# Performance work log

Measured on AMD Instinct MI355X. Metric: run time of the kernel, lower is better.

Reference implementation:

```python
import jax, jax.numpy as jnp
import numpy as np

N, E, H, FE, FV, L, FL, FO = 20000, 320000, 256, 64, 64, 4, 1024, 1


def setup_inputs() -> dict:
    key = jax.random.key(0)
    ks = jax.random.split(key, 28)
    s = 0.05
    rn = lambda k, shp: jax.random.normal(k, shp, jnp.float32) * s
    inp = {
        'x': jax.random.normal(ks[0], (N, FV), jnp.float32),
        'edge_attr': jax.random.normal(ks[1], (E, FE), jnp.float32),
        'edge_index': jax.random.randint(ks[2], (2, E), 0, N, jnp.int64) if False else jax.random.randint(ks[2], (2, E), 0, N),
        'ew': rn(ks[3], (H, FE)), 'eb': rn(ks[4], (H,)),
        'vw': rn(ks[5], (H, FV)), 'vb': rn(ks[6], (H,)),
        'Le_w': rn(ks[7], (L, H, H)), 'Le_b': rn(ks[8], (L, H)),
        'Lv_w': rn(ks[9], (L, H, H)), 'Lv_b': rn(ks[10], (L, H)),
        'bne_g': jnp.ones((L, H), jnp.float32), 'bne_b': jnp.zeros((L, H), jnp.float32),
        'bnv_g': jnp.ones((L, H), jnp.float32), 'bnv_b': jnp.zeros((L, H), jnp.float32),
        'gru_wih': rn(ks[11], (L, 3 * H, H)), 'gru_whh': rn(ks[12], (L, 3 * H, H)),
        'gru_bih': rn(ks[13], (L, 3 * H)), 'gru_bhh': rn(ks[14], (L, 3 * H)),
        'fin_w': rn(ks[15], (FL, H)), 'fin_b': rn(ks[16], (FL,)),
        'out_w': rn(ks[17], (FO, FL)), 'out_b': rn(ks[18], (FO,)),
    }
    return inp


def _bn(x, g, b):
    # BatchNorm1d, training-mode batch statistics (biased variance), eps=1e-5
    m = x.mean(axis=0)
    v = x.var(axis=0)
    return (x - m) * jax.lax.rsqrt(v + 1e-5) * g + b


def _forward(x, edge_attr, edge_index, ew, eb, vw, vb, Le_w, Le_b, Lv_w, Lv_b,
             bne_g, bne_b, bnv_g, bnv_b, gru_wih, gru_whh, gru_bih, gru_bhh,
             fin_w, fin_b, out_w, out_b):
    n_nodes = x.shape[0]
    num_layers = Le_w.shape[0]
    src, dst = edge_index[0], edge_index[1]
    seg = jnp.concatenate([src, dst])  # each edge contributes to both endpoints
    e_in = edge_attr @ ew.T + eb       # [E, H]
    v_in = x @ vw.T + vb               # [N, H]
    for k in range(num_layers):
        e = e_in @ Le_w[k].T + Le_b[k]
        vp = v_in @ Lv_w[k].T + Lv_b[k]
        ep = jax.nn.relu(_bn(e + vp[src] + vp[dst], bne_g[k], bne_b[k]))  # [E, H]
        # scatter-max of incident edge features into each vertex
        vie = jax.ops.segment_max(jnp.concatenate([ep, ep], axis=0), seg,
                                  num_segments=n_nodes)
        vie = jnp.where(jnp.isfinite(vie), vie, 0.0)  # isolated vertices -> 0
        # single-step GRU: input vie, hidden v_in
        gi = vie @ gru_wih[k].T + gru_bih[k]
        gh = v_in @ gru_whh[k].T + gru_bhh[k]
        ir, iz, ig = jnp.split(gi, 3, axis=1)
        hr, hz, hg = jnp.split(gh, 3, axis=1)
        r = jax.nn.sigmoid(ir + hr)
        z = jax.nn.sigmoid(iz + hz)
        n = jnp.tanh(ig + r * hg)
        h = (1.0 - z) * n + z * v_in
        v_c = jax.nn.relu(_bn(h, bnv_g[k], bnv_b[k]))
        v_in = v_c + v_in
        e_in = ep + e_in
    e_fin = e_in @ fin_w.T + fin_b
    return e_fin @ out_w.T + out_b  # [E, 1]


def reference(x, edge_attr, edge_index, ew, eb, vw, vb, Le_w, Le_b, Lv_w, Lv_b,
              bne_g, bne_b, bnv_g, bnv_b, gru_wih, gru_whh, gru_bih, gru_bhh,
              fin_w, fin_b, out_w, out_b):
    return _forward(x, edge_attr, edge_index, ew, eb, vw, vb, Le_w, Le_b, Lv_w,
                    Lv_b, bne_g, bne_b, bnv_g, bnv_b, gru_wih, gru_whh,
                    gru_bih, gru_bhh, fin_w, fin_b, out_w, out_b)
```

## Files before the change

kernel.cpp:

```cpp
#include <hip/hip_runtime.h>
#include <stdint.h>

constexpr int N  = 20000;
constexpr int E  = 320000;
constexpr int H  = 256;
constexpr int FEAT = 64;
constexpr int NL = 4;
constexpr int FL = 1024;
constexpr int NB_E = E / 64;

typedef unsigned short u16;
typedef short bf16x8 __attribute__((ext_vector_type(8)));
typedef float f32x4 __attribute__((ext_vector_type(4)));

__device__ __forceinline__ float bf2f(u16 u) {
    union { uint32_t i; float f; } v; v.i = ((uint32_t)u) << 16; return v.f;
}
__device__ __forceinline__ u16 f2bf(float f) {
    union { uint32_t i; float f; } v; v.f = f;
    uint32_t r = v.i + 0x7FFFu + ((v.i >> 16) & 1u);
    return (u16)(r >> 16);
}
__device__ __forceinline__ float sigmf(float x) { return 1.f / (1.f + __expf(-x)); }
__device__ __forceinline__ float tanhf_(float x) { return 2.f / (1.f + __expf(-2.f * x)) - 1.f; }

__device__ __forceinline__ unsigned int encf(float x) {
    unsigned int u = __float_as_uint(x);
    return (u & 0x80000000u) ? ~u : (u | 0x80000000u);
}
__device__ __forceinline__ float decf(unsigned int k) {
    unsigned int u = (k & 0x80000000u) ? (k ^ 0x80000000u) : ~k;
    return __uint_as_float(u);
}
__device__ __forceinline__ bf16x8 addbf8(bf16x8 a, bf16x8 b) {
    bf16x8 o;
#pragma unroll
    for (int j = 0; j < 8; ++j)
        o[j] = (short)f2bf(bf2f((u16)(unsigned short)a[j]) + bf2f((u16)(unsigned short)b[j]));
    return o;
}

__device__ __forceinline__ bf16x8 ldbf(const float* wf, size_t off) {
    float4 b0 = *(const float4*)(wf + off);
    float4 b1 = *(const float4*)(wf + off + 4);
    bf16x8 r;
    r[0] = (short)f2bf(b0.x); r[1] = (short)f2bf(b0.y);
    r[2] = (short)f2bf(b0.z); r[3] = (short)f2bf(b0.w);
    r[4] = (short)f2bf(b1.x); r[5] = (short)f2bf(b1.y);
    r[6] = (short)f2bf(b1.z); r[7] = (short)f2bf(b1.w);
    return r;
}

__global__ void k_fuse_final(const float* __restrict__ fin_w, const float* __restrict__ fin_b,
                             const float* __restrict__ out_w, const float* __restrict__ out_b,
                             float* __restrict__ w_fo) {
    int h = threadIdx.x;
    float acc = 0.f;
    for (int f = 0; f < FL; ++f) acc = fmaf(out_w[f], fin_w[(size_t)f * H + h], acc);
    w_fo[h] = acc;
    if (h == 0) {
        float b = 0.f;
        for (int f = 0; f < FL; ++f) b = fmaf(out_w[f], fin_b[f], b);
        w_fo[H] = b + out_b[0];
    }
}

__global__ void k_cvt_frag(const float* __restrict__ w, u16* __restrict__ o,
                           int R, int K, int total) {
    int i = blockIdx.x * 256 + threadIdx.x;
    if (i >= total) return;
    int fpm = (R * K) >> 3;
    int m = i / fpm, f = i % fpm;
    int l16 = f & 15, qd = (f >> 4) & 3;
    int rem = f >> 6;
    int kdiv = K >> 5;
    int ks = rem % kdiv, g = rem / kdiv;
    int row = g * 16 + l16, k = ks * 32 + qd * 8;
    const float* src = w + ((size_t)m * R + row) * K + k;
    u16* dst = o + (size_t)i * 8;
    *(ushort4*)dst       = make_ushort4(f2bf(src[0]), f2bf(src[1]), f2bf(src[2]), f2bf(src[3]));
    *(ushort4*)(dst + 4) = make_ushort4(f2bf(src[4]), f2bf(src[5]), f2bf(src[6]), f2bf(src[7]));
}

__global__ void k_zero_int(int* __restrict__ p, int n) {
    int i = blockIdx.x * 256 + threadIdx.x;
    if (i < n) p[i] = 0;
}
__global__ void k_zero_f64(double* __restrict__ p, int n) {
    int i = blockIdx.x * 256 + threadIdx.x;
    if (i < n) p[i] = 0.0;
}
__global__ void k_hist2(const int* __restrict__ src, const int* __restrict__ dst,
                        int* __restrict__ curS, int* __restrict__ curD) {
    int e = blockIdx.x * 256 + threadIdx.x;
    if (e < E) { atomicAdd(&curS[src[e]], 1); atomicAdd(&curD[dst[e]], 1); }
}
__global__ void k_scan(int* __restrict__ cur) {
    __shared__ int cs[256];
    int t = threadIdx.x;
    constexpr int CH = (N + 255) / 256;
    int beg = t * CH, end = min(beg + CH, N);
    int s = 0;
    for (int i = beg; i < end; ++i) s += cur[i];
    cs[t] = s;
    __syncthreads();
    for (int off = 1; off < 256; off <<= 1) {
        int v = cs[t];
        int u = (t >= off) ? cs[t - off] : 0;
        __syncthreads();
        cs[t] = v + u;
        __syncthreads();
    }
    int run = (t > 0) ? cs[t - 1] : 0;
    for (int i = beg; i < end; ++i) { int d = cur[i]; cur[i] = run; run += d; }
}
__global__ void k_fill_perm(const int* __restrict__ src, const int* __restrict__ dst,
                            int* __restrict__ curS, int* __restrict__ curD,
                            int4* __restrict__ adjS, int4* __restrict__ sd2, int* __restrict__ pos) {
    int e = blockIdx.x * 256 + threadIdx.x;
    if (e < E) {
        int s = src[e], d = dst[e];
        int q = atomicAdd(&curD[d], 1);
        sd2[q] = make_int4(s, d, e, 0);
        pos[e] = q;
        int p = atomicAdd(&curS[s], 1);
        adjS[p] = make_int4(q, s, d, s);
    }
}
__global__ void k_fill_u32(unsigned int* __restrict__ p, unsigned int val) {
    size_t i = ((size_t)blockIdx.x * 256 + threadIdx.x) * 4;
    uint4 v = make_uint4(val, val, val, val);
    *(uint4*)(p + i) = v;
}

template <bool W16>
__global__ __launch_bounds__(256, 3) void k_proj_mfma(
    const float* __restrict__ A, const u16* __restrict__ wb, const float* __restrict__ wf,
    const float* __restrict__ bias, u16* __restrict__ C, int M, const int* __restrict__ perm)
{
    __shared__ u16 As[64][72];
    int t = threadIdx.x;
    int row0 = blockIdx.x * 64;
    int r = t >> 2, q = t & 3;
    if (row0 + r < M) {
        const float* gp = A + (size_t)(row0 + r) * FEAT + q * 16;
#pragma unroll
        for (int i = 0; i < 4; ++i) {
            float4 v = *(const float4*)(gp + i * 4);
            *(ushort4*)&As[r][q * 16 + i * 4] = make_ushort4(f2bf(v.x), f2bf(v.y), f2bf(v.z), f2bf(v.w));
        }
    } else {
#pragma unroll
        for (int i = 0; i < 4; ++i) *(ushort4*)&As[r][q * 16 + i * 4] = make_ushort4(0, 0, 0, 0);
    }
    __syncthreads();
    int w = t >> 6, l = t & 63, lane16 = l & 15, quad = l >> 4;
    f32x4 acc[4][4];
#pragma unroll
    for (int i = 0; i < 4; ++i)
#pragma unroll
        for (int j = 0; j < 4; ++j) acc[i][j] = (f32x4){0.f, 0.f, 0.f, 0.f};
    int foff = (quad * 16 + lane16) * 8;
#pragma unroll
    for (int k0 = 0; k0 < FEAT; k0 += 32) {
        int ks = k0 >> 5;
        bf16x8 a[4], b[4];
#pragma unroll
        for (int mt = 0; mt < 4; ++mt)
            a[mt] = *(const bf16x8*)&As[mt * 16 + lane16][k0 + quad * 8];
#pragma unroll
        for (int nt = 0; nt < 4; ++nt) {
            if constexpr (W16)
                b[nt] = *(const bf16x8*)(wb + (size_t)((nt * 4 + w) * 2 + ks) * 512 + foff);
            else
                b[nt] = ldbf(wf, (size_t)(w * 16 + nt * 64 + lane16) * FEAT + k0 + quad * 8);
        }
#pragma unroll
        for (int mt = 0; mt < 4; ++mt)
#pragma unroll
            for (int nt = 0; nt < 4; ++nt)
                acc[mt][nt] = __builtin_amdgcn_mfma_f32_16x16x32_bf16(a[mt], b[nt], acc[mt][nt], 0, 0, 0);
    }
#pragma unroll
    for (int nt = 0; nt < 4; ++nt) {
        int col = w * 16 + nt * 64 + lane16;
        float bv = bias[col];
#pragma unroll
        for (int mt = 0; mt < 4; ++mt)
#pragma unroll
            for (int reg = 0; reg < 4; ++reg) {
                int row = mt * 16 + quad * 4 + reg;
                if (row0 + row < M) {
                    int pr = perm ? perm[row0 + row] : row0 + row;
                    C[(size_t)pr * H + col] = f2bf(acc[mt][nt][reg] + bv);
                }
            }
    }
}

template <bool W16>
__global__ __launch_bounds__(256, 2) void k_node_mfma(
    const u16* __restrict__ A, const u16* __restrict__ wb, const float* __restrict__ wf,
    u16* __restrict__ C)
{
    __shared__ u16 As[64][264];
    int t = threadIdx.x;
    int row0 = blockIdx.x * 64;
    int rows = min(64, N - row0);
    int r = t >> 2, q = t & 3;
    if (r < rows) {
        const u16* gp = A + (size_t)(row0 + r) * H + q * 64;
#pragma unroll
        for (int i = 0; i < 8; ++i)
            *(bf16x8*)&As[r][q * 64 + i * 8] = *(const bf16x8*)(gp + i * 8);
    } else {
#pragma unroll
        for (int i = 0; i < 16; ++i) *(ushort4*)&As[r][q * 64 + i * 4] = make_ushort4(0, 0, 0, 0);
    }
    __syncthreads();
    int w = t >> 6, l = t & 63, lane16 = l & 15, quad = l >> 4;
    f32x4 acc[4][4];
#pragma unroll
    for (int i = 0; i < 4; ++i)
#pragma unroll
        for (int j = 0; j < 4; ++j) acc[i][j] = (f32x4){0.f, 0.f, 0.f, 0.f};
    int foff = (quad * 16 + lane16) * 8;
    for (int k0 = 0; k0 < H; k0 += 32) {
        int ks = k0 >> 5;
        bf16x8 a[4], b[4];
#pragma unroll
        for (int mt = 0; mt < 4; ++mt)
            a[mt] = *(const bf16x8*)&As[mt * 16 + lane16][k0 + quad * 8];
#pragma unroll
        for (int nt = 0; nt < 4; ++nt) {
            if constexpr (W16)
                b[nt] = *(const bf16x8*)(wb + (size_t)((nt * 4 + w) * 8 + ks) * 512 + foff);
            else
                b[nt] = ldbf(wf, (size_t)(w * 16 + nt * 64 + lane16) * H + k0 + quad * 8);
        }
#pragma unroll
        for (int mt = 0; mt < 4; ++mt)
#pragma unroll
            for (int nt = 0; nt < 4; ++nt)
                acc[mt][nt] = __builtin_amdgcn_mfma_f32_16x16x32_bf16(a[mt], b[nt], acc[mt][nt], 0, 0, 0);
    }
#pragma unroll
    for (int nt = 0; nt < 4; ++nt) {
        int col = w * 16 + nt * 64 + lane16;
#pragma unroll
        for (int mt = 0; mt < 4; ++mt)
#pragma unroll
            for (int reg = 0; reg < 4; ++reg) {
                int row = mt * 16 + quad * 4 + reg;
                if (row < rows)
                    C[(size_t)(row0 + row) * H + col] = f2bf(acc[mt][nt][reg]);
            }
    }
}

__global__ __launch_bounds__(512, 4) void k_edge_first(
    const u16* __restrict__ ein2, const u16* __restrict__ wsw,
    const u16* __restrict__ vp, const int4* __restrict__ sd2,
    const int* __restrict__ endo,
    unsigned int* __restrict__ vie, double* __restrict__ stats_e)
{
    __shared__ u16 As[64][264];
    __shared__ u16 Us[64][264];
    __shared__ int s_node[64];
    __shared__ int s_int[64];
    u16 (*praw)[264] = As;

    int t = threadIdx.x;
    int p0 = blockIdx.x * 64;
    int r = t >> 3, q = t & 7;
    {
        int4 en = sd2[p0 + r];
        const u16* gp = ein2 + (size_t)(p0 + r) * H + q * 32;
        const u16* vs = vp + (size_t)en.x * H + q * 32;
        const u16* vd = vp + (size_t)en.y * H + q * 32;
#pragma unroll
        for (int i = 0; i < 4; ++i)
            *(bf16x8*)&As[r][q * 32 + i * 8] = *(const bf16x8*)(gp + i * 8);
#pragma unroll
        for (int i = 0; i < 4; ++i) {
            bf16x8 a8 = *(const bf16x8*)(vs + i * 8);
            bf16x8 b8 = *(const bf16x8*)(vd + i * 8);
            *(bf16x8*)&Us[r][q * 32 + i * 8] = addbf8(a8, b8);
        }
    }
    if (t < 64) {
        int nd = sd2[p0 + t].y;
        s_node[t] = nd;
        int seg0 = p0 + (t & 32);
        int st = (nd == 0) ? 0 : endo[nd - 1];
        int ee = endo[nd];
        s_int[t] = (st >= seg0) && (ee <= seg0 + 32);
    }
    __syncthreads();

    int w = t >> 6, l = t & 63, lane16 = l & 15, quad = l >> 4;
    f32x4 acc[4][2];
#pragma unroll
    for (int i = 0; i < 4; ++i)
#pragma unroll
        for (int j = 0; j < 2; ++j) acc[i][j] = (f32x4){0.f, 0.f, 0.f, 0.f};
    int woff = (quad * 16 + lane16) * 8;
    for (int ks = 0; ks < 8; ++ks) {
        int k0 = ks * 32;
        bf16x8 a[4], b[2];
#pragma unroll
        for (int mt = 0; mt < 4; ++mt)
            a[mt] = *(const bf16x8*)&As[mt * 16 + lane16][k0 + quad * 8];
#pragma unroll
        for (int nt = 0; nt < 2; ++nt)
            b[nt] = *(const bf16x8*)(wsw + (size_t)(w * 2 + nt) * 4096 + ks * 512 + woff);
#pragma unroll
        for (int mt = 0; mt < 4; ++mt)
#pragma unroll
            for (int nt = 0; nt < 2; ++nt)
                acc[mt][nt] = __builtin_amdgcn_mfma_f32_16x16x32_bf16(a[mt], b[nt], acc[mt][nt], 0, 0, 0);
    }
    __syncthreads();

#pragma unroll
    for (int nt = 0; nt < 2; ++nt) {
        int col = w * 32 + nt * 16 + lane16;
        float s = 0.f, qq = 0.f;
#pragma unroll
        for (int mt = 0; mt < 4; ++mt)
#pragma unroll
            for (int reg = 0; reg < 4; ++reg) {
                int row = mt * 16 + quad * 4 + reg;
                float v = acc[mt][nt][reg] + bf2f(Us[row][col]);
                praw[row][col] = f2bf(v);
                s += v; qq += v * v;
            }
        s  += __shfl_xor(s, 16, 64);  s  += __shfl_xor(s, 32, 64);
        qq += __shfl_xor(qq, 16, 64); qq += __shfl_xor(qq, 32, 64);
        if (quad == 0) {
            int slice = blockIdx.x & 63;
            atomicAdd(&stats_e[(size_t)slice * 512 + col], (double)s);
            atomicAdd(&stats_e[(size_t)slice * 512 + 256 + col], (double)qq);
        }
    }
    __syncthreads();
    {
        int seg = t >> 8, col = t & 255;
        int base = seg * 32;
        int cur = s_node[base];
        float m = bf2f(praw[base][col]);
        for (int rr = 1; rr < 32; ++rr) {
            int nd = s_node[base + rr];
            float v = bf2f(praw[base + rr][col]);
            if (nd != cur) {
                if (s_int[base + rr - 1]) vie[(size_t)cur * H + col] = encf(m);
                else atomicMax(&vie[(size_t)cur * H + col], encf(m));
                cur = nd; m = v;
            } else m = fmaxf(m, v);
        }
        if (s_int[base + 31]) vie[(size_t)cur * H + col] = encf(m);
        else atomicMax(&vie[(size_t)cur * H + col], encf(m));
    }
}

__global__ __launch_bounds__(512, 4) void k_edge_second(
    const u16* __restrict__ ein2, const u16* __restrict__ wsw,
    const u16* __restrict__ vp, const int4* __restrict__ adj,
    unsigned int* __restrict__ vie,
    const float* __restrict__ scale, const float* __restrict__ shift,
    u16* __restrict__ ein_rw)
{
    __shared__ u16 As[64][264];
    __shared__ u16 Us[64][264];
    __shared__ int s_pos[64];
    __shared__ int s_node[64];
    u16 (*praw)[264] = As;

    int t = threadIdx.x;
    int p0 = blockIdx.x * 64;
    int r = t >> 3, q = t & 7;
    bf16x8 ein_reg[4];
    {
        int4 en = adj[p0 + r];
        const u16* gp = ein2 + (size_t)en.x * H + q * 32;
        const u16* vs = vp + (size_t)en.y * H + q * 32;
        const u16* vd = vp + (size_t)en.z * H + q * 32;
#pragma unroll
        for (int i = 0; i < 4; ++i) {
            ein_reg[i] = *(const bf16x8*)(gp + i * 8);
            *(bf16x8*)&As[r][q * 32 + i * 8] = ein_reg[i];
        }
#pragma unroll
        for (int i = 0; i < 4; ++i) {
            bf16x8 a8 = *(const bf16x8*)(vs + i * 8);
            bf16x8 b8 = *(const bf16x8*)(vd + i * 8);
            *(bf16x8*)&Us[r][q * 32 + i * 8] = addbf8(a8, b8);
        }
    }
    if (t < 64) {
        int4 en = adj[p0 + t];
        s_pos[t] = en.x; s_node[t] = en.w;
    }
    __syncthreads();

    int w = t >> 6, l = t & 63, lane16 = l & 15, quad = l >> 4;
    f32x4 acc[4][2];
#pragma unroll
    for (int i = 0; i < 4; ++i)
#pragma unroll
        for (int j = 0; j < 2; ++j) acc[i][j] = (f32x4){0.f, 0.f, 0.f, 0.f};
    int woff = (quad * 16 + lane16) * 8;
    for (int ks = 0; ks < 8; ++ks) {
        int k0 = ks * 32;
        bf16x8 a[4], b[2];
#pragma unroll
        for (int mt = 0; mt < 4; ++mt)
            a[mt] = *(const bf16x8*)&As[mt * 16 + lane16][k0 + quad * 8];
#pragma unroll
        for (int nt = 0; nt < 2; ++nt)
            b[nt] = *(const bf16x8*)(wsw + (size_t)(w * 2 + nt) * 4096 + ks * 512 + woff);
#pragma unroll
        for (int mt = 0; mt < 4; ++mt)
#pragma unroll
            for (int nt = 0; nt < 2; ++nt)
                acc[mt][nt] = __builtin_amdgcn_mfma_f32_16x16x32_bf16(a[mt], b[nt], acc[mt][nt], 0, 0, 0);
    }
    __syncthreads();

#pragma unroll
    for (int nt = 0; nt < 2; ++nt) {
        int col = w * 32 + nt * 16 + lane16;
#pragma unroll
        for (int mt = 0; mt < 4; ++mt)
#pragma unroll
            for (int reg = 0; reg < 4; ++reg) {
                int row = mt * 16 + quad * 4 + reg;
                praw[row][col] = f2bf(acc[mt][nt][reg] + bf2f(Us[row][col]));
            }
    }
    __syncthreads();
    {
        int seg = t >> 8, col = t & 255;
        int base = seg * 32;
        int cur = s_node[base];
        float m = bf2f(praw[base][col]);
        for (int rr = 1; rr < 32; ++rr) {
            int nd = s_node[base + rr];
            float v = bf2f(praw[base + rr][col]);
            if (nd != cur) {
                atomicMax(&vie[(size_t)cur * H + col], encf(m));
                cur = nd; m = v;
            } else m = fmaxf(m, v);
        }
        atomicMax(&vie[(size_t)cur * H + col], encf(m));
    }
    {
        u16* gp = ein_rw + (size_t)s_pos[r] * H + q * 32;
        const float* scp = scale + q * 32;
        const float* shp = shift + q * 32;
#pragma unroll
        for (int i = 0; i < 4; ++i) {
            int c = q * 32 + i * 8;
            bf16x8 pr = *(const bf16x8*)&praw[r][c];
            bf16x8 ov;
#pragma unroll
            for (int j = 0; j < 8; ++j) {
                float sc = scp[i * 8 + j];
                float sh = shp[i * 8 + j];
                float o = bf2f((u16)(unsigned short)ein_reg[i][j])
                        + fmaxf(fmaf(bf2f((u16)(unsigned short)pr[j]), sc, sh), 0.f);
                ov[j] = (short)f2bf(o);
            }
            *(bf16x8*)(gp + i * 8) = ov;
        }
    }
}

__global__ void k_bn_final_e(const double* __restrict__ stats_e,
                             const float* __restrict__ g, const float* __restrict__ b,
                             float* __restrict__ scale, float* __restrict__ shift) {
    int j = threadIdx.x;
    double m = 0.0, q = 0.0;
    for (int s = 0; s < 64; ++s) {
        m += stats_e[(size_t)s * 512 + j];
        q += stats_e[(size_t)s * 512 + 256 + j];
    }
    m /= (double)E;
    double var = q / (double)E - m * m;
    if (var < 0.0) var = 0.0;
    float inv = rsqrtf((float)var + 1e-5f);
    float sc = g[j] * inv;
    scale[j] = sc;
    shift[j] = b[j] - (float)m * sc;
}

__global__ void k_bn_final(const double* __restrict__ stats, int base,
                           const float* __restrict__ g, const float* __restrict__ b,
                           double cnt, float* __restrict__ scale, float* __restrict__ shift) {
    int j = threadIdx.x;
    double m = stats[base + j] / cnt;
    double var = stats[base + 256 + j] / cnt - m * m;
    if (var < 0.0) var = 0.0;
    float inv = rsqrtf((float)var + 1e-5f);
    float sc = g[j] * inv;
    scale[j] = sc;
    shift[j] = b[j] - (float)m * sc;
}

__global__ void k_vie_final(unsigned int* __restrict__ vie_u,
                            const float* __restrict__ scale, const float* __restrict__ shift) {
    size_t idx = ((size_t)blockIdx.x * 256 + threadIdx.x) * 4;
    int col = (int)(idx & (size_t)(H - 1));
    uint4 u = *(const uint4*)(vie_u + idx);
    float4 sc = *(const float4*)(scale + col);
    float4 sh = *(const float4*)(shift + col);
    float4 o;
    o.x = (u.x == 0u) ? 0.f : fmaxf(fmaf(decf(u.x), sc.x, sh.x), 0.f);
    o.y = (u.y == 0u) ? 0.f : fmaxf(fmaf(decf(u.y), sc.y, sh.y), 0.f);
    o.z = (u.z == 0u) ? 0.f : fmaxf(fmaf(decf(u.z), sc.z, sh.z), 0.f);
    o.w = (u.w == 0u) ? 0.f : fmaxf(fmaf(decf(u.w), sc.w, sh.w), 0.f);
    *(float4*)((float*)vie_u + idx) = o;
}

template <bool W16>
__global__ __launch_bounds__(256, 3) void k_gru_mfma(
    const float* __restrict__ vie, const u16* __restrict__ vin,
    const u16* __restrict__ wihb, const float* __restrict__ wihf,
    const u16* __restrict__ whhb, const float* __restrict__ whhf,
    const float* __restrict__ bih, const float* __restrict__ bhh,
    u16* __restrict__ hout, double* __restrict__ stats_v)
{
    __shared__ u16 Ae[32][264];
    __shared__ u16 Av[32][264];
    __shared__ float csum[256], csq[256];
    int t = threadIdx.x;
    int row0 = blockIdx.x * 32;
    int rows = min(32, N - row0);
    int r = t >> 3, q = t & 7;
    if (r < rows) {
        const float* gp = vie + (size_t)(row0 + r) * H + q * 32;
        const u16* hp = vin + (size_t)(row0 + r) * H + q * 32;
#pragma unroll
        for (int i = 0; i < 8; ++i) {
            float4 v = *(const float4*)(gp + i * 4);
            *(ushort4*)&Ae[r][q * 32 + i * 4] = make_ushort4(f2bf(v.x), f2bf(v.y), f2bf(v.z), f2bf(v.w));
        }
#pragma unroll
        for (int i = 0; i < 4; ++i)
            *(bf16x8*)&Av[r][q * 32 + i * 8] = *(const bf16x8*)(hp + i * 8);
    } else {
#pragma unroll
        for (int i = 0; i < 8; ++i) {
            *(ushort4*)&Ae[r][q * 32 + i * 4] = make_ushort4(0, 0, 0, 0);
            *(ushort4*)&Av[r][q * 32 + i * 4] = make_ushort4(0, 0, 0, 0);
        }
    }
    __syncthreads();
    int w = t >> 6, l = t & 63, lane16 = l & 15, quad = l >> 4;
    int foff = (quad * 16 + lane16) * 8;

    for (int g = 0; g < 4; ++g) {
        int j = g * 64 + w * 16 + lane16;
        f32x4 aR[2], aZ[2], aIG[2], aHG[2];
#pragma unroll
        for (int mt = 0; mt < 2; ++mt) {
            aR[mt] = (f32x4){0.f, 0.f, 0.f, 0.f};  aZ[mt] = (f32x4){0.f, 0.f, 0.f, 0.f};
            aIG[mt] = (f32x4){0.f, 0.f, 0.f, 0.f}; aHG[mt] = (f32x4){0.f, 0.f, 0.f, 0.f};
        }
        for (int k0 = 0; k0 < H; k0 += 32) {
            bf16x8 ae[2], av[2];
#pragma unroll
            for (int mt = 0; mt < 2; ++mt) {
                ae[mt] = *(const bf16x8*)&Ae[mt * 16 + lane16][k0 + quad * 8];
                av[mt] = *(const bf16x8*)&Av[mt * 16 + lane16][k0 + quad * 8];
            }
            bf16x8 bri, bzi, bgi, brh, bzh, bgh;
            if constexpr (W16) {
                size_t fo = ((size_t)(g * 4 + w) * 8 + (k0 >> 5)) * 512 + foff;
                bri = *(const bf16x8*)(wihb + fo);
                bzi = *(const bf16x8*)(wihb + 65536 + fo);
                bgi = *(const bf16x8*)(wihb + 131072 + fo);
                brh = *(const bf16x8*)(whhb + fo);
                bzh = *(const bf16x8*)(whhb + 65536 + fo);
                bgh = *(const bf16x8*)(whhb + 131072 + fo);
            } else {
                size_t kq = (size_t)k0 + quad * 8;
                bri = ldbf(wihf, (size_t)j * H + kq);
                bzi = ldbf(wihf, (size_t)(H + j) * H + kq);
                bgi = ldbf(wihf, (size_t)(2 * H + j) * H + kq);
                brh = ldbf(whhf, (size_t)j * H + kq);
                bzh = ldbf(whhf, (size_t)(H + j) * H + kq);
                bgh = ldbf(whhf, (size_t)(2 * H + j) * H + kq);
            }
#pragma unroll
            for (int mt = 0; mt < 2; ++mt) {
                aR[mt]  = __builtin_amdgcn_mfma_f32_16x16x32_bf16(ae[mt], bri, aR[mt], 0, 0, 0);
                aR[mt]  = __builtin_amdgcn_mfma_f32_16x16x32_bf16(av[mt], brh, aR[mt], 0, 0, 0);
                aZ[mt]  = __builtin_amdgcn_mfma_f32_16x16x32_bf16(ae[mt], bzi, aZ[mt], 0, 0, 0);
                aZ[mt]  = __builtin_amdgcn_mfma_f32_16x16x32_bf16(av[mt], bzh, aZ[mt], 0, 0, 0);
                aIG[mt] = __builtin_amdgcn_mfma_f32_16x16x32_bf16(ae[mt], bgi, aIG[mt], 0, 0, 0);
                aHG[mt] = __builtin_amdgcn_mfma_f32_16x16x32_bf16(av[mt], bgh, aHG[mt], 0, 0, 0);
            }
        }
        float br_ = bih[j] + bhh[j];
        float bz_ = bih[H + j] + bhh[H + j];
        float bgi_ = bih[2 * H + j];
        float bgh_ = bhh[2 * H + j];
        float s = 0.f, qq = 0.f;
#pragma unroll
        for (int mt = 0; mt < 2; ++mt)
#pragma unroll
            for (int reg = 0; reg < 4; ++reg) {
                int row = mt * 16 + quad * 4 + reg;
                float rr = sigmf(aR[mt][reg] + br_);
                float zz = sigmf(aZ[mt][reg] + bz_);
                float nn = tanhf_(aIG[mt][reg] + bgi_ + rr * (aHG[mt][reg] + bgh_));
                float vv = bf2f(Av[row][j]);
                float hv = (1.f - zz) * nn + zz * vv;
                if (row < rows) {
                    hout[(size_t)(row0 + row) * H + j] = f2bf(hv);
                    s += hv; qq += hv * hv;
                }
            }
        s  += __shfl_xor(s, 16, 64);  s  += __shfl_xor(s, 32, 64);
        qq += __shfl_xor(qq, 16, 64); qq += __shfl_xor(qq, 32, 64);
        if (quad == 0) { csum[j] = s; csq[j] = qq; }
    }
    __syncthreads();
    atomicAdd(&stats_v[t], (double)csum[t]);
    atomicAdd(&stats_v[256 + t], (double)csq[t]);
}

__global__ void k_vertex_update(u16* __restrict__ vin, const u16* __restrict__ h,
                                const float* __restrict__ scale, const float* __restrict__ shift) {
    size_t idx = ((size_t)blockIdx.x * 256 + threadIdx.x) * 4;
    int col = (int)(idx & (size_t)(H - 1));
    ushort4 hv = *(const ushort4*)(h + idx);
    float4 sc = *(const float4*)(scale + col);
    float4 sh = *(const float4*)(shift + col);
    ushort4 vv = *(const ushort4*)(vin + idx);
    float o0 = bf2f(vv.x) + fmaxf(fmaf(bf2f(hv.x), sc.x, sh.x), 0.f);
    float o1 = bf2f(vv.y) + fmaxf(fmaf(bf2f(hv.y), sc.y, sh.y), 0.f);
    float o2 = bf2f(vv.z) + fmaxf(fmaf(bf2f(hv.z), sc.z, sh.z), 0.f);
    float o3 = bf2f(vv.w) + fmaxf(fmaf(bf2f(hv.w), sc.w, sh.w), 0.f);
    *(ushort4*)(vin + idx) = make_ushort4(f2bf(o0), f2bf(o1), f2bf(o2), f2bf(o3));
}

__global__ __launch_bounds__(256) void k_final(const u16* __restrict__ ein2,
                                               const int4* __restrict__ sd2,
                                               const float* __restrict__ w_fo, float* __restrict__ out) {
    int t = threadIdx.x;
    int lane = t & 63;
    int w = (blockIdx.x << 2) + (t >> 6);
    float4 wv = *(const float4*)(w_fo + lane * 4);
    float bfo = w_fo[H];
    int p0 = w * 64;
    for (int p = p0; p < p0 + 64; ++p) {
        ushort4 u = *(const ushort4*)(ein2 + (size_t)p * H + lane * 4);
        float s = bf2f(u.x) * wv.x + bf2f(u.y) * wv.y + bf2f(u.z) * wv.z + bf2f(u.w) * wv.w;
        for (int off = 32; off > 0; off >>= 1) s += __shfl_down(s, off, 64);
        if (lane == 0) out[sd2[p].z] = s + bfo;
    }
}

template <bool W16>
static void run_all(void* const* d_in, void* d_out, void* d_ws, hipStream_t stream) {
    const float* x         = (const float*)d_in[0];
    const float* edge_attr = (const float*)d_in[1];
    const int*   ei        = (const int*)d_in[2];
    const int*   src = ei;
    const int*   dst = ei + E;
    const float* ew  = (const float*)d_in[3];
    const float* eb  = (const float*)d_in[4];
    const float* vw  = (const float*)d_in[5];
    const float* vb  = (const float*)d_in[6];
    const float* Le_w = (const float*)d_in[7];
    const float* Lv_w = (const float*)d_in[9];
    const float* bne_g = (const float*)d_in[11];
    const float* bne_b = (const float*)d_in[12];
    const float* bnv_g = (const float*)d_in[13];
    const float* bnv_b = (const float*)d_in[14];
    const float* gwih  = (const float*)d_in[15];
    const float* gwhh  = (const float*)d_in[16];
    const float* gbih  = (const float*)d_in[17];
    const float* gbhh  = (const float*)d_in[18];
    const float* fin_w = (const float*)d_in[19];
    const float* fin_b = (const float*)d_in[20];
    const float* out_w = (const float*)d_in[21];
    const float* out_b = (const float*)d_in[22];
    float* out = (float*)d_out;

    const size_t nh = (size_t)N * H, eh = (size_t)E * H;
    char* base = (char*)d_ws;
    size_t off = 0;
    auto alloc = [&](size_t bytes) -> char* {
        char* p = base + off;
        off = (off + bytes + 255) & ~(size_t)255;
        return p;
    };
    float* w_fo = (float*)alloc((H + 1) * sizeof(float));
    u16* v_in = (u16*)alloc(nh * sizeof(u16));
    u16* vp   = (u16*)alloc(nh * sizeof(u16));
    unsigned int* vie_u = (unsigned int*)alloc(nh * sizeof(unsigned int));
    u16* e_in = (u16*)alloc(eh * sizeof(u16));
    u16* wbf  = (u16*)alloc((size_t)NL * H * H * sizeof(u16));
    double* stats_e = (double*)alloc((size_t)64 * 512 * sizeof(double));
    double* stats_v = (double*)alloc(512 * sizeof(double));
    float* scale_e = (float*)alloc(H * sizeof(float));
    float* shift_e = (float*)alloc(H * sizeof(float));
    float* scale_v = (float*)alloc(H * sizeof(float));
    float* shift_v = (float*)alloc(H * sizeof(float));
    int* curS = (int*)alloc((size_t)N * sizeof(int));
    int* curD = (int*)alloc((size_t)N * sizeof(int));
    int4* adjS = (int4*)alloc((size_t)E * sizeof(int4));
    int4* sd2  = (int4*)alloc((size_t)E * sizeof(int4));
    int*  pos  = (int*)alloc((size_t)E * sizeof(int));
    u16 *wbf_v = nullptr, *wbf_ih = nullptr, *wbf_hh = nullptr, *ew_b = nullptr, *vw_b = nullptr;
    if (W16) {
        wbf_v  = (u16*)alloc((size_t)NL * H * H * sizeof(u16));
        wbf_ih = (u16*)alloc((size_t)NL * 3 * H * H * sizeof(u16));
        wbf_hh = (u16*)alloc((size_t)NL * 3 * H * H * sizeof(u16));
        ew_b   = (u16*)alloc((size_t)H * FEAT * sizeof(u16));
        vw_b   = (u16*)alloc((size_t)H * FEAT * sizeof(u16));
    }
    u16* hbuf = vp;

    k_fuse_final<<<1, 256, 0, stream>>>(fin_w, fin_b, out_w, out_b, w_fo);
    k_cvt_frag<<<(NL * H * H / 8 + 255) / 256, 256, 0, stream>>>(Le_w, wbf, H, H, NL * H * H / 8);
    if (W16) {
        k_cvt_frag<<<(NL * H * H / 8 + 255) / 256, 256, 0, stream>>>(Lv_w, wbf_v, H, H, NL * H * H / 8);
        k_cvt_frag<<<(NL * 3 * H * H / 8 + 255) / 256, 256, 0, stream>>>(gwih, wbf_ih, H, H, NL * 3 * H * H / 8);
        k_cvt_frag<<<(NL * 3 * H * H / 8 + 255) / 256, 256, 0, stream>>>(gwhh, wbf_hh, H, H, NL * 3 * H * H / 8);
        k_cvt_frag<<<(H * FEAT / 8 + 255) / 256, 256, 0, stream>>>(ew, ew_b, H, FEAT, H * FEAT / 8);
        k_cvt_frag<<<(H * FEAT / 8 + 255) / 256, 256, 0, stream>>>(vw, vw_b, H, FEAT, H * FEAT / 8);
    }
    k_zero_int<<<(N + 255) / 256, 256, 0, stream>>>(curS, N);
    k_zero_int<<<(N + 255) / 256, 256, 0, stream>>>(curD, N);
    k_hist2<<<E / 256, 256, 0, stream>>>(src, dst, curS, curD);
    k_scan<<<1, 256, 0, stream>>>(curS);
    k_scan<<<1, 256, 0, stream>>>(curD);
    k_fill_perm<<<E / 256, 256, 0, stream>>>(src, dst, curS, curD, adjS, sd2, pos);
    const int ntile = (N + 63) / 64;
    k_proj_mfma<W16><<<ntile, 256, 0, stream>>>(x, vw_b, vw, vb, v_in, N, nullptr);
    k_proj_mfma<W16><<<E / 64, 256, 0, stream>>>(edge_attr, ew_b, ew, eb, e_in, E, pos);

    const int nstat = 64 * 512 + 512;
    const int gtile = (N + 31) / 32;
    for (int k = 0; k < NL; ++k) {
        k_zero_f64<<<(nstat + 255) / 256, 256, 0, stream>>>(stats_e, nstat);
        k_fill_u32<<<(int)(nh / 4 / 256), 256, 0, stream>>>(vie_u, 0u);
        k_node_mfma<W16><<<ntile, 256, 0, stream>>>(v_in,
            W16 ? wbf_v + (size_t)k * H * H : nullptr, Lv_w + (size_t)k * H * H, vp);
        k_edge_first<<<NB_E, 512, 0, stream>>>(e_in, wbf + (size_t)k * H * H, vp,
                                               sd2, curD, vie_u, stats_e);
        k_bn_final_e<<<1, 256, 0, stream>>>(stats_e, bne_g + k * H, bne_b + k * H, scale_e, shift_e);
        k_edge_second<<<NB_E, 512, 0, stream>>>(e_in, wbf + (size_t)k * H * H, vp,
                                                adjS, vie_u, scale_e, shift_e, e_in);
        k_vie_final<<<(int)(nh / 4 / 256), 256, 0, stream>>>(vie_u, scale_e, shift_e);
        k_gru_mfma<W16><<<gtile, 256, 0, stream>>>((const float*)vie_u, v_in,
            W16 ? wbf_ih + (size_t)k * 3 * H * H : nullptr, gwih + (size_t)k * 3 * H * H,
            W16 ? wbf_hh + (size_t)k * 3 * H * H : nullptr, gwhh + (size_t)k * 3 * H * H,
            gbih + (size_t)k * 3 * H, gbhh + (size_t)k * 3 * H, hbuf, stats_v);
        k_bn_final<<<1, 256, 0, stream>>>(stats_v, 0, bnv_g + k * H, bnv_b + k * H, (double)N, scale_v, shift_v);
        k_vertex_update<<<(int)(nh / 4 / 256), 256, 0, stream>>>(v_in, hbuf, scale_v, shift_v);
    }
    k_final<<<E / 256, 256, 0, stream>>>(e_in, sd2, w_fo, out);
}

extern "C" void kernel_launch(void* const* d_in, const int* in_sizes, int n_in,
                              void* d_out, int out_size, void* d_ws, size_t ws_size,
                              hipStream_t stream) {
    (void)in_sizes; (void)n_in; (void)out_size;
    const size_t nh = (size_t)N * H, eh = (size_t)E * H;
    auto rup = [](size_t x) { return (x + 255) & ~(size_t)255; };
    size_t need_base = rup((H + 1) * 4) + 2 * rup(nh * 2) + rup(nh * 4) + rup(eh * 2)
                     + rup((size_t)NL * H * H * 2) + rup((size_t)64 * 512 * 8) + rup(512 * 8)
                     + 4 * rup(H * 4) + 2 * rup((size_t)N * 4) + 2 * rup((size_t)E * 16)
                     + rup((size_t)E * 4);
    size_t need_w16 = rup((size_t)NL * H * H * 2)
                    + 2 * rup((size_t)NL * 3 * H * H * 2) + 2 * rup((size_t)H * FEAT * 2);
    if (ws_size == 0 || ws_size >= need_base + need_w16)
        run_all<true>(d_in, d_out, d_ws, stream);
    else
        run_all<false>(d_in, d_out, d_ws, stream);
}
```

Before: 2.467 ms.

## Make edge kernels persistent over several tiles, keeping half the weights in registers

Both edge kernels now process ET=5 consecutive 64-edge tiles per block, with the grid shrunk to match. Half of each wave's weight fragment is loaded into registers once and reused across tiles, and the other half is still read from global memory each k-step. This cuts block launch overhead and repeated weight loads, but adds register pressure under launch_bounds(512,4) and one extra barrier per tile. Fewer blocks (1000) also means less latency hiding from block-level parallelism.

```diff
diff --git a/kernel.cpp b/kernel.cpp
--- a/kernel.cpp
+++ b/kernel.cpp
@@ -8,6 +8,7 @@
 constexpr int NL = 4;
 constexpr int FL = 1024;
 constexpr int NB_E = E / 64;
+constexpr int ET = 5;
 
 typedef unsigned short u16;
 typedef short bf16x8 __attribute__((ext_vector_type(8)));
@@ -271,95 +272,105 @@
     u16 (*praw)[264] = As;
 
     int t = threadIdx.x;
-    int p0 = blockIdx.x * 64;
     int r = t >> 3, q = t & 7;
-    {
-        int4 en = sd2[p0 + r];
-        const u16* gp = ein2 + (size_t)(p0 + r) * H + q * 32;
-        const u16* vs = vp + (size_t)en.x * H + q * 32;
-        const u16* vd = vp + (size_t)en.y * H + q * 32;
+    int w = t >> 6, l = t & 63, lane16 = l & 15, quad = l >> 4;
+    int woff = (quad * 16 + lane16) * 8;
+
+    bf16x8 wreg0[8];
+#pragma unroll
+    for (int ks = 0; ks < 8; ++ks)
+        wreg0[ks] = *(const bf16x8*)(wsw + (size_t)(w * 2) * 4096 + ks * 512 + woff);
+    const u16* wb1 = wsw + (size_t)(w * 2 + 1) * 4096 + woff;
+
+    for (int it = 0; it < ET; ++it) {
+        int tile = blockIdx.x * ET + it;
+        int p0 = tile * 64;
+        {
+            int4 en = sd2[p0 + r];
+            const u16* gp = ein2 + (size_t)(p0 + r) * H + q * 32;
+            const u16* vs = vp + (size_t)en.x * H + q * 32;
+            const u16* vd = vp + (size_t)en.y * H + q * 32;
+#pragma unroll
+            for (int i = 0; i < 4; ++i)
+                *(bf16x8*)&As[r][q * 32 + i * 8] = *(const bf16x8*)(gp + i * 8);
+#pragma unroll
+            for (int i = 0; i < 4; ++i) {
+                bf16x8 a8 = *(const bf16x8*)(vs + i * 8);
+                bf16x8 b8 = *(const bf16x8*)(vd + i * 8);
+                *(bf16x8*)&Us[r][q * 32 + i * 8] = addbf8(a8, b8);
+            }
+        }
+        if (t < 64) {
+            int nd = sd2[p0 + t].y;
+            s_node[t] = nd;
+            int seg0 = p0 + (t & 32);
+            int st = (nd == 0) ? 0 : endo[nd - 1];
+            int ee = endo[nd];
+            s_int[t] = (st >= seg0) && (ee <= seg0 + 32);
+        }
+        __syncthreads();
+
+        f32x4 acc[4][2];
 #pragma unroll
         for (int i = 0; i < 4; ++i)
-            *(bf16x8*)&As[r][q * 32 + i * 8] = *(const bf16x8*)(gp + i * 8);
-#pragma unroll
-        for (int i = 0; i < 4; ++i) {
-            bf16x8 a8 = *(const bf16x8*)(vs + i * 8);
-            bf16x8 b8 = *(const bf16x8*)(vd + i * 8);
-            *(bf16x8*)&Us[r][q * 32 + i * 8] = addbf8(a8, b8);
-        }
-    }
-    if (t < 64) {
-        int nd = sd2[p0 + t].y;
-        s_node[t] = nd;
-        int seg0 = p0 + (t & 32);
-        int st = (nd == 0) ? 0 : endo[nd - 1];
-        int ee = endo[nd];
-        s_int[t] = (st >= seg0) && (ee <= seg0 + 32);
-    }
-    __syncthreads();
-
-    int w = t >> 6, l = t & 63, lane16 = l & 15, quad = l >> 4;
-    f32x4 acc[4][2];
-#pragma unroll
-    for (int i = 0; i < 4; ++i)
-#pragma unroll
-        for (int j = 0; j < 2; ++j) acc[i][j] = (f32x4){0.f, 0.f, 0.f, 0.f};
-    int woff = (quad * 16 + lane16) * 8;
-    for (int ks = 0; ks < 8; ++ks) {
-        int k0 = ks * 32;
-        bf16x8 a[4], b[2];
-#pragma unroll
-        for (int mt = 0; mt < 4; ++mt)
-            a[mt] = *(const bf16x8*)&As[mt * 16 + lane16][k0 + quad * 8];
-#pragma unroll
-        for (int nt = 0; nt < 2; ++nt)
-            b[nt] = *(const bf16x8*)(wsw + (size_t)(w * 2 + nt) * 4096 + ks * 512 + woff);
-#pragma unroll
-        for (int mt = 0; mt < 4; ++mt)
-#pragma unroll
-            for (int nt = 0; nt < 2; ++nt)
-                acc[mt][nt] = __builtin_amdgcn_mfma_f32_16x16x32_bf16(a[mt], b[nt], acc[mt][nt], 0, 0, 0);
-    }
-    __syncthreads();
-
-#pragma unroll
-    for (int nt = 0; nt < 2; ++nt) {
-        int col = w * 32 + nt * 16 + lane16;
-        float s = 0.f, qq = 0.f;
-#pragma unroll
-        for (int mt = 0; mt < 4; ++mt)
-#pragma unroll
-            for (int reg = 0; reg < 4; ++reg) {
-                int row = mt * 16 + quad * 4 + reg;
-                float v = acc[mt][nt][reg] + bf2f(Us[row][col]);
-                praw[row][col] = f2bf(v);
-                s += v; qq += v * v;
-            }
-        s  += __shfl_xor(s, 16, 64);  s  += __shfl_xor(s, 32, 64);
-        qq += __shfl_xor(qq, 16, 64); qq += __shfl_xor(qq, 32, 64);
-        if (quad == 0) {
-            int slice = blockIdx.x & 63;
-            atomicAdd(&stats_e[(size_t)slice * 512 + col], (double)s);
-            atomicAdd(&stats_e[(size_t)slice * 512 + 256 + col], (double)qq);
-        }
-    }
-    __syncthreads();
-    {
-        int seg = t >> 8, col = t & 255;
-        int base = seg * 32;
-        int cur = s_node[base];
-        float m = bf2f(praw[base][col]);
-        for (int rr = 1; rr < 32; ++rr) {
-            int nd = s_node[base + rr];
-            float v = bf2f(praw[base + rr][col]);
-            if (nd != cur) {
-                if (s_int[base + rr - 1]) vie[(size_t)cur * H + col] = encf(m);
-                else atomicMax(&vie[(size_t)cur * H + col], encf(m));
-                cur = nd; m = v;
-            } else m = fmaxf(m, v);
-        }
-        if (s_int[base + 31]) vie[(size_t)cur * H + col] = encf(m);
-        else atomicMax(&vie[(size_t)cur * H + col], encf(m));
+#pragma unroll
+            for (int j = 0; j < 2; ++j) acc[i][j] = (f32x4){0.f, 0.f, 0.f, 0.f};
+#pragma unroll
+        for (int ks = 0; ks < 8; ++ks) {
+            int k0 = ks * 32;
+            bf16x8 a[4];
+#pragma unroll
+            for (int mt = 0; mt < 4; ++mt)
+                a[mt] = *(const bf16x8*)&As[mt * 16 + lane16][k0 + quad * 8];
+            bf16x8 b1 = *(const bf16x8*)(wb1 + ks * 512);
+#pragma unroll
+            for (int mt = 0; mt < 4; ++mt) {
+                acc[mt][0] = __builtin_amdgcn_mfma_f32_16x16x32_bf16(a[mt], wreg0[ks], acc[mt][0], 0, 0, 0);
+                acc[mt][1] = __builtin_amdgcn_mfma_f32_16x16x32_bf16(a[mt], b1, acc[mt][1], 0, 0, 0);
+            }
+        }
+        __syncthreads();
+
+#pragma unroll
+        for (int nt = 0; nt < 2; ++nt) {
+            int col = w * 32 + nt * 16 + lane16;
+            float s = 0.f, qq = 0.f;
+#pragma unroll
+            for (int mt = 0; mt < 4; ++mt)
+#pragma unroll
+                for (int reg = 0; reg < 4; ++reg) {
+                    int row = mt * 16 + quad * 4 + reg;
+                    float v = acc[mt][nt][reg] + bf2f(Us[row][col]);
+                    praw[row][col] = f2bf(v);
+                    s += v; qq += v * v;
+                }
+            s  += __shfl_xor(s, 16, 64);  s  += __shfl_xor(s, 32, 64);
+            qq += __shfl_xor(qq, 16, 64); qq += __shfl_xor(qq, 32, 64);
+            if (quad == 0) {
+                int slice = tile & 63;
+                atomicAdd(&stats_e[(size_t)slice * 512 + col], (double)s);
+                atomicAdd(&stats_e[(size_t)slice * 512 + 256 + col], (double)qq);
+            }
+        }
+        __syncthreads();
+        {
+            int seg = t >> 8, col = t & 255;
+            int base = seg * 32;
+            int cur = s_node[base];
+            float m = bf2f(praw[base][col]);
+            for (int rr = 1; rr < 32; ++rr) {
+                int nd = s_node[base + rr];
+                float v = bf2f(praw[base + rr][col]);
+                if (nd != cur) {
+                    if (s_int[base + rr - 1]) vie[(size_t)cur * H + col] = encf(m);
+                    else atomicMax(&vie[(size_t)cur * H + col], encf(m));
+                    cur = nd; m = v;
+                } else m = fmaxf(m, v);
+            }
+            if (s_int[base + 31]) vie[(size_t)cur * H + col] = encf(m);
+            else atomicMax(&vie[(size_t)cur * H + col], encf(m));
+        }
+        __syncthreads();
     }
 }
 
@@ -377,102 +388,111 @@
     u16 (*praw)[264] = As;
 
     int t = threadIdx.x;
-    int p0 = blockIdx.x * 64;
     int r = t >> 3, q = t & 7;
-    bf16x8 ein_reg[4];
-    {
-        int4 en = adj[p0 + r];
-        const u16* gp = ein2 + (size_t)en.x * H + q * 32;
-        const u16* vs = vp + (size_t)en.y * H + q * 32;
-        const u16* vd = vp + (size_t)en.z * H + q * 32;
-#pragma unroll
-        for (int i = 0; i < 4; ++i) {
-            ein_reg[i] = *(const bf16x8*)(gp + i * 8);
-            *(bf16x8*)&As[r][q * 32 + i * 8] = ein_reg[i];
-        }
-#pragma unroll
-        for (int i = 0; i < 4; ++i) {
-            bf16x8 a8 = *(const bf16x8*)(vs + i * 8);
-            bf16x8 b8 = *(const bf16x8*)(vd + i * 8);
-            *(bf16x8*)&Us[r][q * 32 + i * 8] = addbf8(a8, b8);
-        }
-    }
-    if (t < 64) {
-        int4 en = adj[p0 + t];
-        s_pos[t] = en.x; s_node[t] = en.w;
-    }
-    __syncthreads();
-
     int w = t >> 6, l = t & 63, lane16 = l & 15, quad = l >> 4;
-    f32x4 acc[4][2];
-#pragma unroll
-    for (int i = 0; i < 4; ++i)
-#pragma unroll
-        for (int j = 0; j < 2; ++j) acc[i][j] = (f32x4){0.f, 0.f, 0.f, 0.f};
     int woff = (quad * 16 + lane16) * 8;
-    for (int ks = 0; ks < 8; ++ks) {
-        int k0 = ks * 32;
-        bf16x8 a[4], b[2];
-#pragma unroll
-        for (int mt = 0; mt < 4; ++mt)
-            a[mt] = *(const bf16x8*)&As[mt * 16 + lane16][k0 + quad * 8];
-#pragma unroll
-        for (int nt = 0; nt < 2; ++nt)
-            b[nt] = *(const bf16x8*)(wsw + (size_t)(w * 2 + nt) * 4096 + ks * 512 + woff);
-#pragma unroll
-        for (int mt = 0; mt < 4; ++mt)
-#pragma unroll
-            for (int nt = 0; nt < 2; ++nt)
-                acc[mt][nt] = __builtin_amdgcn_mfma_f32_16x16x32_bf16(a[mt], b[nt], acc[mt][nt], 0, 0, 0);
-    }
-    __syncthreads();
-
-#pragma unroll
-    for (int nt = 0; nt < 2; ++nt) {
-        int col = w * 32 + nt * 16 + lane16;
-#pragma unroll
-        for (int mt = 0; mt < 4; ++mt)
-#pragma unroll
-            for (int reg = 0; reg < 4; ++reg) {
-                int row = mt * 16 + quad * 4 + reg;
-                praw[row][col] = f2bf(acc[mt][nt][reg] + bf2f(Us[row][col]));
-            }
-    }
-    __syncthreads();
-    {
-        int seg = t >> 8, col = t & 255;
-        int base = seg * 32;
-        int cur = s_node[base];
-        float m = bf2f(praw[base][col]);
-        for (int rr = 1; rr < 32; ++rr) {
-            int nd = s_node[base + rr];
-            float v = bf2f(praw[base + rr][col]);
-            if (nd != cur) {
-                atomicMax(&vie[(size_t)cur * H + col], encf(m));
-                cur = nd; m = v;
-            } else m = fmaxf(m, v);
-        }
-        atomicMax(&vie[(size_t)cur * H + col], encf(m));
-    }
-    {
-        u16* gp = ein_rw + (size_t)s_pos[r] * H + q * 32;
-        const float* scp = scale + q * 32;
-        const float* shp = shift + q * 32;
-#pragma unroll
-        for (int i = 0; i < 4; ++i) {
-            int c = q * 32 + i * 8;
-            bf16x8 pr = *(const bf16x8*)&praw[r][c];
-            bf16x8 ov;
-#pragma unroll
-            for (int j = 0; j < 8; ++j) {
-                float sc = scp[i * 8 + j];
-                float sh = shp[i * 8 + j];
-                float o = bf2f((u16)(unsigned short)ein_reg[i][j])
-                        + fmaxf(fmaf(bf2f((u16)(unsigned short)pr[j]), sc, sh), 0.f);
-                ov[j] = (short)f2bf(o);
-            }
-            *(bf16x8*)(gp + i * 8) = ov;
-        }
+
+    bf16x8 wreg0[8];
+#pragma unroll
+    for (int ks = 0; ks < 8; ++ks)
+        wreg0[ks] = *(const bf16x8*)(wsw + (size_t)(w * 2) * 4096 + ks * 512 + woff);
+    const u16* wb1 = wsw + (size_t)(w * 2 + 1) * 4096 + woff;
+
+    for (int it = 0; it < ET; ++it) {
+        int p0 = (blockIdx.x * ET + it) * 64;
+        bf16x8 ein_reg[4];
+        {
+            int4 en = adj[p0 + r];
+            const u16* gp = ein2 + (size_t)en.x * H + q * 32;
+            const u16* vs = vp + (size_t)en.y * H + q * 32;
+            const u16* vd = vp + (size_t)en.z * H + q * 32;
+#pragma unroll
+            for (int i = 0; i < 4; ++i) {
+                ein_reg[i] = *(const bf16x8*)(gp + i * 8);
+                *(bf16x8*)&As[r][q * 32 + i * 8] = ein_reg[i];
+            }
+#pragma unroll
+            for (int i = 0; i < 4; ++i) {
+                bf16x8 a8 = *(const bf16x8*)(vs + i * 8);
+                bf16x8 b8 = *(const bf16x8*)(vd + i * 8);
+                *(bf16x8*)&Us[r][q * 32 + i * 8] = addbf8(a8, b8);
+            }
+        }
+        if (t < 64) {
+            int4 en = adj[p0 + t];
+            s_pos[t] = en.x; s_node[t] = en.w;
+        }
+        __syncthreads();
+
+        f32x4 acc[4][2];
+#pragma unroll
+        for (int i = 0; i < 4; ++i)
+#pragma unroll
+            for (int j = 0; j < 2; ++j) acc[i][j] = (f32x4){0.f, 0.f, 0.f, 0.f};
+#pragma unroll
+        for (int ks = 0; ks < 8; ++ks) {
+            int k0 = ks * 32;
+            bf16x8 a[4];
+#pragma unroll
+            for (int mt = 0; mt < 4; ++mt)
+                a[mt] = *(const bf16x8*)&As[mt * 16 + lane16][k0 + quad * 8];
+            bf16x8 b1 = *(const bf16x8*)(wb1 + ks * 512);
+#pragma unroll
+            for (int mt = 0; mt < 4; ++mt) {
+                acc[mt][0] = __builtin_amdgcn_mfma_f32_16x16x32_bf16(a[mt], wreg0[ks], acc[mt][0], 0, 0, 0);
+                acc[mt][1] = __builtin_amdgcn_mfma_f32_16x16x32_bf16(a[mt], b1, acc[mt][1], 0, 0, 0);
+            }
+        }
+        __syncthreads();
+
+#pragma unroll
+        for (int nt = 0; nt < 2; ++nt) {
+            int col = w * 32 + nt * 16 + lane16;
+#pragma unroll
+            for (int mt = 0; mt < 4; ++mt)
+#pragma unroll
+                for (int reg = 0; reg < 4; ++reg) {
+                    int row = mt * 16 + quad * 4 + reg;
+                    praw[row][col] = f2bf(acc[mt][nt][reg] + bf2f(Us[row][col]));
+                }
+        }
+        __syncthreads();
+        {
+            int seg = t >> 8, col = t & 255;
+            int base = seg * 32;
+            int cur = s_node[base];
+            float m = bf2f(praw[base][col]);
+            for (int rr = 1; rr < 32; ++rr) {
+                int nd = s_node[base + rr];
+                float v = bf2f(praw[base + rr][col]);
+                if (nd != cur) {
+                    atomicMax(&vie[(size_t)cur * H + col], encf(m));
+                    cur = nd; m = v;
+                } else m = fmaxf(m, v);
+            }
+            atomicMax(&vie[(size_t)cur * H + col], encf(m));
+        }
+        {
+            u16* gp = ein_rw + (size_t)s_pos[r] * H + q * 32;
+            const float* scp = scale + q * 32;
+            const float* shp = shift + q * 32;
+#pragma unroll
+            for (int i = 0; i < 4; ++i) {
+                int c = q * 32 + i * 8;
+                bf16x8 pr = *(const bf16x8*)&praw[r][c];
+                bf16x8 ov;
+#pragma unroll
+                for (int j = 0; j < 8; ++j) {
+                    float sc = scp[i * 8 + j];
+                    float sh = shp[i * 8 + j];
+                    float o = bf2f((u16)(unsigned short)ein_reg[i][j])
+                            + fmaxf(fmaf(bf2f((u16)(unsigned short)pr[j]), sc, sh), 0.f);
+                    ov[j] = (short)f2bf(o);
+                }
+                *(bf16x8*)(gp + i * 8) = ov;
+            }
+        }
+        __syncthreads();
     }
 }
 
@@ -751,11 +771,11 @@
         k_fill_u32<<<(int)(nh / 4 / 256), 256, 0, stream>>>(vie_u, 0u);
         k_node_mfma<W16><<<ntile, 256, 0, stream>>>(v_in,
             W16 ? wbf_v + (size_t)k * H * H : nullptr, Lv_w + (size_t)k * H * H, vp);
-        k_edge_first<<<NB_E, 512, 0, stream>>>(e_in, wbf + (size_t)k * H * H, vp,
-                                               sd2, curD, vie_u, stats_e);
+        k_edge_first<<<NB_E / ET, 512, 0, stream>>>(e_in, wbf + (size_t)k * H * H, vp,
+                                                    sd2, curD, vie_u, stats_e);
         k_bn_final_e<<<1, 256, 0, stream>>>(stats_e, bne_g + k * H, bne_b + k * H, scale_e, shift_e);
-        k_edge_second<<<NB_E, 512, 0, stream>>>(e_in, wbf + (size_t)k * H * H, vp,
-                                                adjS, vie_u, scale_e, shift_e, e_in);
+        k_edge_second<<<NB_E / ET, 512, 0, stream>>>(e_in, wbf + (size_t)k * H * H, vp,
+                                                     adjS, vie_u, scale_e, shift_e, e_in);
         k_vie_final<<<(int)(nh / 4 / 256), 256, 0, stream>>>(vie_u, scale_e, shift_e);
         k_gru_mfma<W16><<<gtile, 256, 0, stream>>>((const float*)vie_u, v_in,
             W16 ? wbf_ih + (size_t)k * 3 * H * H : nullptr, gwih + (size_t)k * 3 * H * H,
```

Measured after the change: 2.950 ms. 19.6% more time.
